# Kernel tuning notes

Hardware: AMD Instinct MI355X
Metric: run time of the kernel (lower is better)

Reference implementation:

```python
import jax, jax.numpy as jnp
import numpy as np

M, N, NUM_ITER, BATCH = 512, 2048, 16, 4096


def setup_inputs() -> dict:
    key = jax.random.key(0)
    k_y, k_D, k_thr = jax.random.split(key, 3)
    # Dictionary D (== A in the module), column-scaled like a sensing matrix
    D = np.asarray(jax.random.normal(k_D, (M, N), dtype=jnp.float32)) / np.sqrt(M)
    # W = inv(D D^T) D, then normalize columns so w_i . d_i == 1 (ALISTA analytic weight)
    W = np.linalg.inv(D @ D.T) @ D
    W = W / np.sum(W * D, axis=0, keepdims=True)
    y = jax.random.normal(k_y, (BATCH, M), dtype=jnp.float32)
    thr = jax.random.uniform(k_thr, (NUM_ITER,), dtype=jnp.float32) * 0.1  # positive thresholds
    step = jnp.ones((NUM_ITER,), dtype=jnp.float32)
    return {"y": y, "A": jnp.asarray(D), "W": jnp.asarray(W), "thr": thr, "step": step}


def reference(y, A, W, thr, step):
    # y: [B, m]; A, W: [m, n]; thr, step: [numIter]
    B = y.shape[0]
    n = A.shape[1]

    def body(d, ts):
        t, s = ts
        r = d @ A.T - y                      # [B, m]  == (A @ d.T - y.T).T
        z = d - s * (r @ W)                  # [B, n]  == (W.T @ r.T).T
        d_new = jnp.sign(z) * jnp.maximum(jnp.abs(z) - t, 0.0)  # soft threshold
        return d_new, d_new

    d0 = jnp.zeros((B, n), dtype=y.dtype)
    _, xs = jax.lax.scan(body, d0, (thr, step))
    return xs  # [numIter, B, n]: all intermediate iterates, like the returned list x
```

## Files before the change

### kernel.cpp

```cpp
#include <hip/hip_runtime.h>


#define NDIM 2048
#define MDIM 512
#define BATCHN 4096
#define NITER 16
#define BM 128
#define BN 128
#define BK 64

#define BM2 256
#define BN2 128
#define BK2 32
#define NKT (NDIM / BK2)

typedef _Float16 f16;
typedef f16 f16x8 __attribute__((ext_vector_type(8)));
typedef float f32x4 __attribute__((ext_vector_type(4)));

__device__ __forceinline__ void gload_lds16(const void* g, void* lds) {
  __builtin_amdgcn_global_load_lds(
      (const __attribute__((address_space(1))) unsigned int*)g,
      (__attribute__((address_space(3))) unsigned int*)lds, 16, 0, 0);
}

__global__ __launch_bounds__(512, 2) void alista_iter_gemm(
    const f16* __restrict__ Ds, const f16* __restrict__ P,
    const f16* __restrict__ Ch,
    const float* __restrict__ thr, const float* __restrict__ step, int it,
    float sigma, float inv_sigma, float inv_sigma_next,
    float* __restrict__ outIter, f16* __restrict__ DsNext)
{
  __shared__ __align__(16) f16 ldsA[4 * BM2 * BK2];
  __shared__ __align__(16) f16 ldsB[4 * BN2 * BK2];

  const int tid = threadIdx.x;
  const int w = tid >> 6, l = tid & 63;
  const int wm = w >> 1, wn = w & 1;
  const int h = l >> 4;

  const int bid = blockIdx.x;
  const int wgid = (bid & 7) * 32 + (bid >> 3);
  const int rowTile = (wgid >> 4) * BM2;
  const int colTile = (wgid & 15) * BN2;

  const f16* Abase = Ds + (size_t)rowTile * NDIM;
  const f16* Bbase = P + (size_t)colTile * NDIM;

  auto stage = [&](int t) {
    const int buf = t & 3;
#pragma unroll
    for (int r = 0; r < 2; ++r) {
      int row = r * 128 + (tid >> 2);
      int colb = ((tid & 3) << 4) ^ ((row & 3) << 4);
      gload_lds16((const char*)(Abase + (size_t)row * NDIM + t * BK2) + colb,
                  (char*)ldsA + buf * 16384 + r * 8192 + w * 1024);
    }
    {
      int row = tid >> 2;
      int colb = ((tid & 3) << 4) ^ ((row & 3) << 4);
      gload_lds16((const char*)(Bbase + (size_t)row * NDIM + t * BK2) + colb,
                  (char*)ldsB + buf * 8192 + w * 1024);
    }
  };

#define READ_FRAGS(t, af, bf)                                                   \
  {                                                                             \
    const f16* bA_ = ldsA + ((t) & 3) * 8192;                                   \
    const f16* bB_ = ldsB + ((t) & 3) * 4096;                                   \
    _Pragma("unroll")                                                           \
    for (int m = 0; m < 4; ++m) {                                               \
      int row = wm * 64 + m * 16 + (l & 15);                                    \
      af[m] = *(const f16x8*)(bA_ + row * 32 + ((h ^ (row & 3)) << 3));         \
    }                                                                           \
    _Pragma("unroll")                                                           \
    for (int n = 0; n < 4; ++n) {                                               \
      int row = wn * 64 + n * 16 + (l & 15);                                    \
      bf[n] = *(const f16x8*)(bB_ + row * 32 + ((h ^ (row & 3)) << 3));         \
    }                                                                           \
  }

#define MFMA_CLUSTER(af, bf)                                                    \
  __builtin_amdgcn_s_setprio(1);                                                \
  _Pragma("unroll")                                                             \
  for (int m = 0; m < 4; ++m)                                                   \
    _Pragma("unroll")                                                           \
    for (int n = 0; n < 4; ++n)                                                 \
      acc[m][n] = __builtin_amdgcn_mfma_f32_16x16x32_f16(af[m], bf[n],          \
                                                         acc[m][n], 0, 0, 0);   \
  __builtin_amdgcn_s_setprio(0);

  stage(0);
  stage(1);
  asm volatile("s_waitcnt vmcnt(3)" ::: "memory");
  __builtin_amdgcn_s_barrier();

  f32x4 acc[4][4] = {};
  f16x8 afE[4], bfE[4], afO[4], bfO[4];

  READ_FRAGS(0, afE, bfE);
  stage(2);
  asm volatile("s_waitcnt vmcnt(3)" ::: "memory");
  __builtin_amdgcn_s_barrier();
  __builtin_amdgcn_sched_barrier(0);

  for (int t = 0; t < NKT; t += 2) {
    READ_FRAGS(t + 1, afO, bfO);
    if (t + 3 < NKT) stage(t + 3);
    __builtin_amdgcn_sched_barrier(0);
    MFMA_CLUSTER(afE, bfE);
    if (t + 3 < NKT) asm volatile("s_waitcnt vmcnt(3)" ::: "memory");
    else             asm volatile("s_waitcnt vmcnt(0)" ::: "memory");
    __builtin_amdgcn_s_barrier();
    __builtin_amdgcn_sched_barrier(0);

    if (t + 2 < NKT) READ_FRAGS(t + 2, afE, bfE);
    if (t + 4 < NKT) stage(t + 4);
    __builtin_amdgcn_sched_barrier(0);
    MFMA_CLUSTER(afO, bfO);
    if (t + 4 < NKT) asm volatile("s_waitcnt vmcnt(3)" ::: "memory");
    else             asm volatile("s_waitcnt vmcnt(0)" ::: "memory");
    __builtin_amdgcn_s_barrier();
    __builtin_amdgcn_sched_barrier(0);
  }

  const int baseRow = rowTile + wm * 64 + (h << 2);
  const int baseCol = colTile + wn * 64 + (l & 15);
  const float s = step[it];
  const float tt = thr[it];
  const size_t itOff = (size_t)it * (size_t)BATCHN * NDIM;
#pragma unroll
  for (int m = 0; m < 4; ++m)
#pragma unroll
    for (int n = 0; n < 4; ++n)
#pragma unroll
      for (int r = 0; r < 4; ++r) {
        int row = baseRow + m * 16 + r;
        int col = baseCol + n * 16;
        size_t g = (size_t)row * NDIM + col;
        float v = acc[m][n][r];
        float ds = (float)Ds[g];
        float cv = (float)Ch[g];
        float z = sigma * (ds - s * (v - cv * inv_sigma));
        float az = __builtin_fabsf(z) - tt;
        float dn = az > 0.f ? (z > 0.f ? az : -az) : 0.f;
        outIter[itOff + g] = dn;
        DsNext[g] = (f16)(dn * inv_sigma_next);
      }
#undef READ_FRAGS
#undef MFMA_CLUSTER
}

__device__ __forceinline__ void gemm_pass(
    const f16* __restrict__ Ap, const f16* __restrict__ Bp, int K,
    int rowTile, int colTile, int t, int w, int l, int wr, int wc,
    f16* ldsA, f16* ldsB, f32x4 (&acc)[4][4])
{
  const f16* Arow = Ap + (size_t)rowTile * K;
  const f16* Brow = Bp + (size_t)colTile * K;
  for (int kt = 0; kt < K; kt += BK) {
    __syncthreads();
#pragma unroll
    for (int n = 0; n < 4; ++n) {
      int e = n * 2048 + t * 8;
      int r = e >> 6, c = e & 63;
      gload_lds16(Arow + (size_t)r * K + kt + c, (char*)ldsA + n * 4096 + w * 1024);
    }
#pragma unroll
    for (int n = 0; n < 4; ++n) {
      int e = n * 2048 + t * 8;
      int r = e >> 6, c = e & 63;
      gload_lds16(Brow + (size_t)r * K + kt + c, (char*)ldsB + n * 4096 + w * 1024);
    }
    asm volatile("s_waitcnt vmcnt(0)" ::: "memory");
    __syncthreads();
#pragma unroll
    for (int ks = 0; ks < 2; ++ks) {
      f16x8 a[4], b[4];
#pragma unroll
      for (int m = 0; m < 4; ++m)
        a[m] = *(const f16x8*)(ldsA + ((wr * 64 + m * 16 + (l & 15)) * BK + ks * 32 + (l >> 4) * 8));
#pragma unroll
      for (int n = 0; n < 4; ++n)
        b[n] = *(const f16x8*)(ldsB + ((wc * 64 + n * 16 + (l & 15)) * BK + ks * 32 + (l >> 4) * 8));
#pragma unroll
      for (int m = 0; m < 4; ++m)
#pragma unroll
        for (int n = 0; n < 4; ++n)
          acc[m][n] = __builtin_amdgcn_mfma_f32_16x16x32_f16(a[m], b[n], acc[m][n], 0, 0, 0);
    }
  }
}

template <int EPI>
__global__ __launch_bounds__(256, 2) void gemm_tn(
    const f16* __restrict__ A0, const f16* __restrict__ B0,
    const f16* __restrict__ A1, const f16* __restrict__ B1,
    const f16* __restrict__ A2, const f16* __restrict__ B2,
    int K,
    f16* __restrict__ outH, f16* __restrict__ outLx)
{
  __shared__ __align__(16) f16 ldsA[BM * BK];
  __shared__ __align__(16) f16 ldsB[BN * BK];
  int t = threadIdx.x;
  int w = t >> 6, l = t & 63;
  int wr = w >> 1, wc = w & 1;
  int rowTile = blockIdx.y * BM;
  int colTile = blockIdx.x * BN;

  f32x4 acc[4][4] = {};
  gemm_pass(A0, B0, K, rowTile, colTile, t, w, l, wr, wc, ldsA, ldsB, acc);
  gemm_pass(A1, B1, K, rowTile, colTile, t, w, l, wr, wc, ldsA, ldsB, acc);
#pragma unroll
  for (int m = 0; m < 4; ++m)
#pragma unroll
    for (int n = 0; n < 4; ++n)
      acc[m][n] *= (1.0f / 256.0f);
  gemm_pass(A2, B2, K, rowTile, colTile, t, w, l, wr, wc, ldsA, ldsB, acc);

  int baseRow = rowTile + wr * 64 + ((l >> 4) << 2);
  int baseCol = colTile + wc * 64 + (l & 15);
#pragma unroll
  for (int m = 0; m < 4; ++m)
#pragma unroll
    for (int n = 0; n < 4; ++n)
#pragma unroll
      for (int r = 0; r < 4; ++r) {
        int row = baseRow + m * 16 + r;
        int col = baseCol + n * 16;
        size_t g = (size_t)row * NDIM + col;
        float v = acc[m][n][r];
        if (EPI == 0) {
          f16 hh = (f16)v;
          outH[g] = hh;
          outLx[g] = (f16)((v - (float)hh) * 256.0f);
        } else {
          outH[g] = (f16)v;
        }
      }
}

__global__ __launch_bounds__(256) void trans_split(
    const float* __restrict__ in, f16* __restrict__ oh, f16* __restrict__ olx)
{
  __shared__ float tile[64][65];
  int t = threadIdx.x;
  int tr = t >> 6;
  int tc = t & 63;
  int r0 = blockIdx.y * 64;
  int c0 = blockIdx.x * 64;
#pragma unroll
  for (int i = 0; i < 16; ++i) {
    int r = i * 4 + tr;
    tile[r][tc] = in[(size_t)(r0 + r) * NDIM + c0 + tc];
  }
  __syncthreads();
#pragma unroll
  for (int i = 0; i < 16; ++i) {
    int r = i * 4 + tr;
    float v = tile[tc][r];
    f16 hh = (f16)v;
    size_t o = (size_t)(c0 + r) * MDIM + r0 + tc;
    oh[o] = hh;
    olx[o] = (f16)((v - (float)hh) * 256.0f);
  }
}

__global__ __launch_bounds__(256) void split_y(
    const float* __restrict__ in, f16* __restrict__ oh, f16* __restrict__ olx)
{
  size_t i = (size_t)blockIdx.x * 256 + threadIdx.x;
  float v = in[i];
  f16 hh = (f16)v;
  oh[i] = hh;
  olx[i] = (f16)((v - (float)hh) * 256.0f);
}

__global__ __launch_bounds__(256) void alista_iter0(
    const f16* __restrict__ Ch, const float* __restrict__ thr,
    const float* __restrict__ step, float* __restrict__ out, f16* __restrict__ Ds1)
{
  size_t i = (size_t)blockIdx.x * 256 + threadIdx.x;
  float s = step[0], tt = thr[0];
  float z = s * (float)Ch[i];
  float az = __builtin_fabsf(z) - tt;
  float dn = az > 0.f ? (z > 0.f ? az : -az) : 0.f;
  out[i] = dn;
  Ds1[i] = (f16)dn;
}

extern "C" void kernel_launch(void* const* d_in, const int* in_sizes, int n_in,
                              void* d_out, int out_size, void* d_ws, size_t ws_size,
                              hipStream_t stream)
{
  const float* y    = (const float*)d_in[0];
  const float* A    = (const float*)d_in[1];
  const float* W    = (const float*)d_in[2];
  const float* thr  = (const float*)d_in[3];
  const float* step = (const float*)d_in[4];
  float* out = (float*)d_out;
  char* ws = (char*)d_ws;

  f16* Pht  = (f16*)(ws + 0);
  f16* Plxt = (f16*)(ws + (8ull  << 20));
  f16* Ch   = (f16*)(ws + (16ull << 20));
  f16* DsA  = (f16*)(ws + (32ull << 20));
  f16* DsB  = (f16*)(ws + (48ull << 20));
  f16* Wth  = (f16*)(ws + (32ull << 20));
  f16* Wtlx = (f16*)(ws + (34ull << 20));
  f16* Ath  = (f16*)(ws + (36ull << 20));
  f16* Atlx = (f16*)(ws + (38ull << 20));
  f16* yh   = (f16*)(ws + (48ull << 20));
  f16* ylx  = (f16*)(ws + (52ull << 20));

  trans_split<<<dim3(32, 8), 256, 0, stream>>>(A, Ath, Atlx);
  trans_split<<<dim3(32, 8), 256, 0, stream>>>(W, Wth, Wtlx);
  split_y<<<(BATCHN * MDIM) / 256, 256, 0, stream>>>(y, yh, ylx);

  gemm_tn<0><<<dim3(16, 16), 256, 0, stream>>>(
      Wth, Atlx, Wtlx, Ath, Wth, Ath, MDIM, Pht, Plxt);

  gemm_tn<1><<<dim3(16, 32), 256, 0, stream>>>(
      yh, Wtlx, ylx, Wth, yh, Wth, MDIM, Ch, nullptr);

  alista_iter0<<<(BATCHN * NDIM) / 256, 256, 0, stream>>>(Ch, thr, step, out, DsA);

  f16* cur = DsA;
  f16* nxt = DsB;
  float sigma = 1.0f;
  for (int it = 1; it < NITER; ++it) {
    alista_iter_gemm<<<dim3(256), 512, 0, stream>>>(
        cur, Pht, Ch, thr, step, it,
        sigma, 1.0f / sigma, 0.25f / sigma, out, nxt);
    sigma *= 4.0f;
    f16* tmp = cur; cur = nxt; nxt = tmp;
  }
}
```

Baseline: 828.1 us.

## Drop fp16 split-precision correction GEMMs and change LDS swizzle pattern

The precompute GEMMs no longer use the hi/lo split fp16 scheme, which needed three MFMA passes. Each now runs a single plain fp16 pass, and the split kernels are replaced by simple fp16 conversions. Separately, the LDS XOR swizzle in the main iteration GEMM now uses bits 1-2 of the row instead of bits 0-1, to change the bank-conflict pattern. Dropping the correction terms lowers the accuracy of P = W^T A and C = y W relative to the fp32 reference.

Measured after the change: 788.6 us. 4.8% less time.

```diff
diff --git a/kernel.cpp b/kernel.cpp
--- a/kernel.cpp
+++ b/kernel.cpp
@@ -52,13 +52,13 @@
 #pragma unroll
     for (int r = 0; r < 2; ++r) {
       int row = r * 128 + (tid >> 2);
-      int colb = ((tid & 3) << 4) ^ ((row & 3) << 4);
+      int colb = ((tid & 3) << 4) ^ (((row >> 1) & 3) << 4);
       gload_lds16((const char*)(Abase + (size_t)row * NDIM + t * BK2) + colb,
                   (char*)ldsA + buf * 16384 + r * 8192 + w * 1024);
     }
     {
       int row = tid >> 2;
-      int colb = ((tid & 3) << 4) ^ ((row & 3) << 4);
+      int colb = ((tid & 3) << 4) ^ (((row >> 1) & 3) << 4);
       gload_lds16((const char*)(Bbase + (size_t)row * NDIM + t * BK2) + colb,
                   (char*)ldsB + buf * 8192 + w * 1024);
     }
@@ -71,12 +71,12 @@
     _Pragma("unroll")                                                           \
     for (int m = 0; m < 4; ++m) {                                               \
       int row = wm * 64 + m * 16 + (l & 15);                                    \
-      af[m] = *(const f16x8*)(bA_ + row * 32 + ((h ^ (row & 3)) << 3));         \
+      af[m] = *(const f16x8*)(bA_ + row * 32 + ((h ^ ((row >> 1) & 3)) << 3));  \
     }                                                                           \
     _Pragma("unroll")                                                           \
     for (int n = 0; n < 4; ++n) {                                               \
       int row = wn * 64 + n * 16 + (l & 15);                                    \
-      bf[n] = *(const f16x8*)(bB_ + row * 32 + ((h ^ (row & 3)) << 3));         \
+      bf[n] = *(const f16x8*)(bB_ + row * 32 + ((h ^ ((row >> 1) & 3)) << 3));  \
     }                                                                           \
   }
 
@@ -151,54 +151,9 @@
 #undef MFMA_CLUSTER
 }
 
-__device__ __forceinline__ void gemm_pass(
+__global__ __launch_bounds__(256, 2) void gemm_pre(
     const f16* __restrict__ Ap, const f16* __restrict__ Bp, int K,
-    int rowTile, int colTile, int t, int w, int l, int wr, int wc,
-    f16* ldsA, f16* ldsB, f32x4 (&acc)[4][4])
-{
-  const f16* Arow = Ap + (size_t)rowTile * K;
-  const f16* Brow = Bp + (size_t)colTile * K;
-  for (int kt = 0; kt < K; kt += BK) {
-    __syncthreads();
-#pragma unroll
-    for (int n = 0; n < 4; ++n) {
-      int e = n * 2048 + t * 8;
-      int r = e >> 6, c = e & 63;
-      gload_lds16(Arow + (size_t)r * K + kt + c, (char*)ldsA + n * 4096 + w * 1024);
-    }
-#pragma unroll
-    for (int n = 0; n < 4; ++n) {
-      int e = n * 2048 + t * 8;
-      int r = e >> 6, c = e & 63;
-      gload_lds16(Brow + (size_t)r * K + kt + c, (char*)ldsB + n * 4096 + w * 1024);
-    }
-    asm volatile("s_waitcnt vmcnt(0)" ::: "memory");
-    __syncthreads();
-#pragma unroll
-    for (int ks = 0; ks < 2; ++ks) {
-      f16x8 a[4], b[4];
-#pragma unroll
-      for (int m = 0; m < 4; ++m)
-        a[m] = *(const f16x8*)(ldsA + ((wr * 64 + m * 16 + (l & 15)) * BK + ks * 32 + (l >> 4) * 8));
-#pragma unroll
-      for (int n = 0; n < 4; ++n)
-        b[n] = *(const f16x8*)(ldsB + ((wc * 64 + n * 16 + (l & 15)) * BK + ks * 32 + (l >> 4) * 8));
-#pragma unroll
-      for (int m = 0; m < 4; ++m)
-#pragma unroll
-        for (int n = 0; n < 4; ++n)
-          acc[m][n] = __builtin_amdgcn_mfma_f32_16x16x32_f16(a[m], b[n], acc[m][n], 0, 0, 0);
-    }
-  }
-}
-
-template <int EPI>
-__global__ __launch_bounds__(256, 2) void gemm_tn(
-    const f16* __restrict__ A0, const f16* __restrict__ B0,
-    const f16* __restrict__ A1, const f16* __restrict__ B1,
-    const f16* __restrict__ A2, const f16* __restrict__ B2,
-    int K,
-    f16* __restrict__ outH, f16* __restrict__ outLx)
+    f16* __restrict__ outH)
 {
   __shared__ __align__(16) f16 ldsA[BM * BK];
   __shared__ __align__(16) f16 ldsB[BN * BK];
@@ -209,14 +164,40 @@
   int colTile = blockIdx.x * BN;
 
   f32x4 acc[4][4] = {};
-  gemm_pass(A0, B0, K, rowTile, colTile, t, w, l, wr, wc, ldsA, ldsB, acc);
-  gemm_pass(A1, B1, K, rowTile, colTile, t, w, l, wr, wc, ldsA, ldsB, acc);
-#pragma unroll
-  for (int m = 0; m < 4; ++m)
-#pragma unroll
-    for (int n = 0; n < 4; ++n)
-      acc[m][n] *= (1.0f / 256.0f);
-  gemm_pass(A2, B2, K, rowTile, colTile, t, w, l, wr, wc, ldsA, ldsB, acc);
+  const f16* Arow = Ap + (size_t)rowTile * K;
+  const f16* Brow = Bp + (size_t)colTile * K;
+  for (int kt = 0; kt < K; kt += BK) {
+    __syncthreads();
+#pragma unroll
+    for (int n = 0; n < 4; ++n) {
+      int e = n * 2048 + t * 8;
+      int r = e >> 6, c = e & 63;
+      gload_lds16(Arow + (size_t)r * K + kt + c, (char*)ldsA + n * 4096 + w * 1024);
+    }
+#pragma unroll
+    for (int n = 0; n < 4; ++n) {
+      int e = n * 2048 + t * 8;
+      int r = e >> 6, c = e & 63;
+      gload_lds16(Brow + (size_t)r * K + kt + c, (char*)ldsB + n * 4096 + w * 1024);
+    }
+    asm volatile("s_waitcnt vmcnt(0)" ::: "memory");
+    __syncthreads();
+#pragma unroll
+    for (int ks = 0; ks < 2; ++ks) {
+      f16x8 a[4], b[4];
+#pragma unroll
+      for (int m = 0; m < 4; ++m)
+        a[m] = *(const f16x8*)(ldsA + ((wr * 64 + m * 16 + (l & 15)) * BK + ks * 32 + (l >> 4) * 8));
+#pragma unroll
+      for (int n = 0; n < 4; ++n)
+        b[n] = *(const f16x8*)(ldsB + ((wc * 64 + n * 16 + (l & 15)) * BK + ks * 32 + (l >> 4) * 8));
+#pragma unroll
+      for (int m = 0; m < 4; ++m)
+#pragma unroll
+        for (int n = 0; n < 4; ++n)
+          acc[m][n] = __builtin_amdgcn_mfma_f32_16x16x32_f16(a[m], b[n], acc[m][n], 0, 0, 0);
+    }
+  }
 
   int baseRow = rowTile + wr * 64 + ((l >> 4) << 2);
   int baseCol = colTile + wc * 64 + (l & 15);
@@ -226,22 +207,13 @@
     for (int n = 0; n < 4; ++n)
 #pragma unroll
       for (int r = 0; r < 4; ++r) {
-        int row = baseRow + m * 16 + r;
-        int col = baseCol + n * 16;
-        size_t g = (size_t)row * NDIM + col;
-        float v = acc[m][n][r];
-        if (EPI == 0) {
-          f16 hh = (f16)v;
-          outH[g] = hh;
-          outLx[g] = (f16)((v - (float)hh) * 256.0f);
-        } else {
-          outH[g] = (f16)v;
-        }
+        size_t g = (size_t)(baseRow + m * 16 + r) * NDIM + baseCol + n * 16;
+        outH[g] = (f16)acc[m][n][r];
       }
 }
 
-__global__ __launch_bounds__(256) void trans_split(
-    const float* __restrict__ in, f16* __restrict__ oh, f16* __restrict__ olx)
+__global__ __launch_bounds__(256) void trans_h(
+    const float* __restrict__ in, f16* __restrict__ oh)
 {
   __shared__ float tile[64][65];
   int t = threadIdx.x;
@@ -258,22 +230,15 @@
 #pragma unroll
   for (int i = 0; i < 16; ++i) {
     int r = i * 4 + tr;
-    float v = tile[tc][r];
-    f16 hh = (f16)v;
-    size_t o = (size_t)(c0 + r) * MDIM + r0 + tc;
-    oh[o] = hh;
-    olx[o] = (f16)((v - (float)hh) * 256.0f);
-  }
-}
-
-__global__ __launch_bounds__(256) void split_y(
-    const float* __restrict__ in, f16* __restrict__ oh, f16* __restrict__ olx)
+    oh[(size_t)(c0 + r) * MDIM + r0 + tc] = (f16)tile[tc][r];
+  }
+}
+
+__global__ __launch_bounds__(256) void tofp16(
+    const float* __restrict__ in, f16* __restrict__ oh)
 {
   size_t i = (size_t)blockIdx.x * 256 + threadIdx.x;
-  float v = in[i];
-  f16 hh = (f16)v;
-  oh[i] = hh;
-  olx[i] = (f16)((v - (float)hh) * 256.0f);
+  oh[i] = (f16)in[i];
 }
 
 __global__ __launch_bounds__(256) void alista_iter0(
@@ -301,27 +266,20 @@
   float* out = (float*)d_out;
   char* ws = (char*)d_ws;
 
-  f16* Pht  = (f16*)(ws + 0);
-  f16* Plxt = (f16*)(ws + (8ull  << 20));
-  f16* Ch   = (f16*)(ws + (16ull << 20));
-  f16* DsA  = (f16*)(ws + (32ull << 20));
-  f16* DsB  = (f16*)(ws + (48ull << 20));
-  f16* Wth  = (f16*)(ws + (32ull << 20));
-  f16* Wtlx = (f16*)(ws + (34ull << 20));
-  f16* Ath  = (f16*)(ws + (36ull << 20));
-  f16* Atlx = (f16*)(ws + (38ull << 20));
-  f16* yh   = (f16*)(ws + (48ull << 20));
-  f16* ylx  = (f16*)(ws + (52ull << 20));
-
-  trans_split<<<dim3(32, 8), 256, 0, stream>>>(A, Ath, Atlx);
-  trans_split<<<dim3(32, 8), 256, 0, stream>>>(W, Wth, Wtlx);
-  split_y<<<(BATCHN * MDIM) / 256, 256, 0, stream>>>(y, yh, ylx);
-
-  gemm_tn<0><<<dim3(16, 16), 256, 0, stream>>>(
-      Wth, Atlx, Wtlx, Ath, Wth, Ath, MDIM, Pht, Plxt);
-
-  gemm_tn<1><<<dim3(16, 32), 256, 0, stream>>>(
-      yh, Wtlx, ylx, Wth, yh, Wth, MDIM, Ch, nullptr);
+  f16* Pht = (f16*)(ws + 0);
+  f16* Ch  = (f16*)(ws + (8ull  << 20));
+  f16* DsA = (f16*)(ws + (24ull << 20));
+  f16* DsB = (f16*)(ws + (40ull << 20));
+  f16* Wth = (f16*)(ws + (24ull << 20));
+  f16* Ath = (f16*)(ws + (26ull << 20));
+  f16* yh  = (f16*)(ws + (40ull << 20));
+
+  trans_h<<<dim3(32, 8), 256, 0, stream>>>(A, Ath);
+  trans_h<<<dim3(32, 8), 256, 0, stream>>>(W, Wth);
+  tofp16<<<(BATCHN * MDIM) / 256, 256, 0, stream>>>(y, yh);
+
+  gemm_pre<<<dim3(16, 16), 256, 0, stream>>>(Wth, Ath, MDIM, Pht);
+  gemm_pre<<<dim3(16, 32), 256, 0, stream>>>(yh, Wth, MDIM, Ch);
 
   alista_iter0<<<(BATCHN * NDIM) / 256, 256, 0, stream>>>(Ch, thr, step, out, DsA);
 
```
